# Kernel optimization log

Measured on AMD Instinct MI355X. Metric: run time of the kernel, lower is better.

## Reference

```python
import jax, jax.numpy as jnp
import numpy as np

B, C, H, Wd = 16, 256, 64, 64
D_MODEL = 256


def setup_inputs() -> dict:
    key = jax.random.key(0)
    kx, kw = jax.random.split(key)
    x = jax.random.normal(kx, (B, C, H, Wd), dtype=jnp.float32)
    # 1x1 conv weight [out_c=1+2*d_model, in_c], scaled like kaiming-ish init
    W = jax.random.normal(kw, (1 + 2 * D_MODEL, C), dtype=jnp.float32) / np.sqrt(C)
    return {"x": x, "W": W}


def reference(x, W):
    b, c, h, w = x.shape
    d = (W.shape[0] - 1) // 2
    n = h * w
    xf = x.reshape(b, c, n)                      # [b, c, N]
    qkv = jnp.einsum('oc,bcn->bon', W, xf)       # 1x1 conv == channel GEMM
    q = qkv[:, :1]                               # [b, 1, N]
    k = qkv[:, 1:1 + d]                          # [b, d, N]
    v = qkv[:, 1 + d:]                           # [b, d, N]
    scores = jax.nn.softmax(q, axis=-1)          # softmax over tokens
    ctx = jnp.sum(k * scores, axis=-1, keepdims=True)  # [b, d, 1]
    out = jax.nn.relu(v) * ctx                   # gated ReLU(v)
    return out.reshape(b, d, h, w)
```

## Files before the change

kernel.cpp:

```cpp
#include <hip/hip_runtime.h>
#include <cstdint>
#include <cstddef>

#define NB 16
#define NC 256
#define NN 4096
#define ND 256

typedef unsigned short u16;
typedef unsigned int u32;

typedef __attribute__((ext_vector_type(8))) short short8;
typedef __attribute__((ext_vector_type(4))) float f32x4;

__device__ __forceinline__ u16 f2bf(float f) {
  union { float f; u32 u; } v; v.f = f;
  u32 r = v.u + 0x7FFFu + ((v.u >> 16) & 1u);
  return (u16)(r >> 16);
}
__device__ __forceinline__ float bf2f(u16 h) {
  union { u32 u; float f; } v; v.u = ((u32)h) << 16; return v.f;
}

__global__ __launch_bounds__(256) void k_fuse1(const float* __restrict__ x,
                                               const float* __restrict__ W,
                                               u16* __restrict__ xbT,
                                               u16* __restrict__ wvb,
                                               float* __restrict__ pm,
                                               float* __restrict__ pl,
                                               float* __restrict__ pacc) {
  __shared__ float qred[32 * 65];
  __shared__ float qred2[4 * 65];
  const int t = threadIdx.x;
  const int b = blockIdx.y, n0 = blockIdx.x * 64;
  const int tx = t & 7, ty = t >> 3;
  const int c0 = ty * 8, nl = tx * 8;
  const float* xb = x + (size_t)b * NC * NN + n0;

  const float4 w0 = *(const float4*)(W + c0);
  const float4 w1 = *(const float4*)(W + c0 + 4);
  const float wq[8] = {w0.x, w0.y, w0.z, w0.w, w1.x, w1.y, w1.z, w1.w};

  short8 pk[8];
  float qp[8] = {0.f, 0.f, 0.f, 0.f, 0.f, 0.f, 0.f, 0.f};

#pragma unroll
  for (int r = 0; r < 8; ++r) {
    const float* xr = xb + (size_t)(c0 + r) * NN + nl;
    const float4 va = *(const float4*)(xr);
    const float4 vb = *(const float4*)(xr + 4);
    qp[0] += wq[r] * va.x; qp[1] += wq[r] * va.y;
    qp[2] += wq[r] * va.z; qp[3] += wq[r] * va.w;
    qp[4] += wq[r] * vb.x; qp[5] += wq[r] * vb.y;
    qp[6] += wq[r] * vb.z; qp[7] += wq[r] * vb.w;
    pk[0][r] = (short)f2bf(va.x); pk[1][r] = (short)f2bf(va.y);
    pk[2][r] = (short)f2bf(va.z); pk[3][r] = (short)f2bf(va.w);
    pk[4][r] = (short)f2bf(vb.x); pk[5][r] = (short)f2bf(vb.y);
    pk[6][r] = (short)f2bf(vb.z); pk[7][r] = (short)f2bf(vb.w);
  }

  u16* ob = xbT + (size_t)(b * NN + n0 + nl) * NC + c0;
#pragma unroll
  for (int j = 0; j < 8; ++j)
    *(short8*)(ob + (size_t)j * NC) = pk[j];

#pragma unroll
  for (int j = 0; j < 8; ++j) qred[ty * 65 + nl + j] = qp[j];
  __syncthreads();
  {
    const int n = t & 63, g = t >> 6;
    float s = 0.f;
#pragma unroll
    for (int k = 0; k < 8; ++k) s += qred[(g * 8 + k) * 65 + n];
    qred2[g * 65 + n] = s;
  }
  __syncthreads();

  float q[8];
#pragma unroll
  for (int j = 0; j < 8; ++j)
    q[j] = qred2[0 * 65 + nl + j] + qred2[1 * 65 + nl + j] +
           qred2[2 * 65 + nl + j] + qred2[3 * 65 + nl + j];

  float m = q[0];
#pragma unroll
  for (int j = 1; j < 8; ++j) m = fmaxf(m, q[j]);
#pragma unroll
  for (int off = 1; off < 8; off <<= 1) m = fmaxf(m, __shfl_xor(m, off));

  float p[8]; float l = 0.f;
#pragma unroll
  for (int j = 0; j < 8; ++j) { p[j] = __expf(q[j] - m); l += p[j]; }
#pragma unroll
  for (int off = 1; off < 8; off <<= 1) l += __shfl_xor(l, off);

  float sc[8];
#pragma unroll
  for (int r = 0; r < 8; ++r) {
    float s = 0.f;
#pragma unroll
    for (int j = 0; j < 8; ++j) s += bf2f((u16)pk[j][r]) * p[j];
    sc[r] = s;
  }
#pragma unroll
  for (int off = 1; off < 8; off <<= 1) {
#pragma unroll
    for (int r = 0; r < 8; ++r) sc[r] += __shfl_xor(sc[r], off);
  }
  if (tx == 0) {
    float* pp = pacc + ((size_t)b * 64 + blockIdx.x) * NC + c0;
#pragma unroll
    for (int r = 0; r < 8; ++r) pp[r] = sc[r];
  }
  if (t == 0) {
    pm[b * 64 + blockIdx.x] = m;
    pl[b * 64 + blockIdx.x] = l;
  }

  if (b == 0 && blockIdx.x < 8) {
    const float* wv = W + (size_t)(1 + ND) * NC;
    const int base = blockIdx.x * 8192;
#pragma unroll
    for (int i = 0; i < 8; ++i) {
      const int idx = base + i * 1024 + t * 4;
      const float4 v = *(const float4*)(wv + idx);
      ushort4 o = {f2bf(v.x), f2bf(v.y), f2bf(v.z), f2bf(v.w)};
      *(ushort4*)(wvb + idx) = o;
    }
  }
}

#define BM 128
#define BN 128
#define BK 64

__global__ __launch_bounds__(256, 4) void k_gemm(const u16* __restrict__ xbT,
                                                 const u16* __restrict__ wvb,
                                                 const float* __restrict__ W,
                                                 const float* __restrict__ pm,
                                                 const float* __restrict__ pl,
                                                 const float* __restrict__ pacc,
                                                 float* __restrict__ out) {
  __shared__ __align__(16) u16 As[BM * BK];
  __shared__ __align__(16) u16 Bs[BN * BK];
  __shared__ float am[64], al[64];
  __shared__ __align__(16) float sx[NC];
  __shared__ float sctx[NC];

  const int t = threadIdx.x;
  const int d0 = blockIdx.x * BM;
  const int n0 = blockIdx.y * BN;
  const int b = blockIdx.z;
  const int lane = t & 63, w = t >> 6;
  const int wd = (w & 1) * 64, wn = (w >> 1) * 64;
  const int quad = lane >> 4, l15 = lane & 15;

  const int rstg = t >> 3;
  const int l8 = ((t & 7) ^ (rstg & 7)) * 8;
  const u16* gA = wvb + (size_t)(d0 + rstg) * NC + l8;
  const u16* gB = xbT + (size_t)(b * NN + n0 + rstg) * NC + l8;
  const int ldst = 8 * t;

#pragma unroll
  for (int i = 0; i < 4; ++i) {
    __builtin_amdgcn_global_load_lds(
        (const __attribute__((address_space(1))) u32*)(gA + (size_t)(32 * i) * NC),
        (__attribute__((address_space(3))) u32*)(As + 2048 * i + ldst), 16, 0, 0);
    __builtin_amdgcn_global_load_lds(
        (const __attribute__((address_space(1))) u32*)(gB + (size_t)(32 * i) * NC),
        (__attribute__((address_space(3))) u32*)(Bs + 2048 * i + ldst), 16, 0, 0);
  }

  if (t < 64) { am[t] = pm[b * 64 + t]; al[t] = pl[b * 64 + t]; }
  __syncthreads();
  float M2 = -3.4e38f;
#pragma unroll
  for (int i = 0; i < 64; ++i) M2 = fmaxf(M2, am[i]);
  {
    float xsv = 0.f, L2s = 0.f;
#pragma unroll 8
    for (int i = 0; i < 64; ++i) {
      const float wgt = __expf(am[i] - M2);
      L2s += wgt * al[i];
      xsv += wgt * pacc[(size_t)(b * 64 + i) * NC + t];
    }
    sx[t] = xsv / L2s;
  }
  __syncthreads();
  {
    const float* wk = W + (size_t)(1 + t) * NC;
    float a = 0.f;
#pragma unroll 4
    for (int c4 = 0; c4 < 64; ++c4) {
      const float4 w4 = *(const float4*)(wk + c4 * 4);
      const float4 s4 = *(const float4*)&sx[c4 * 4];
      a += w4.x * s4.x + w4.y * s4.y + w4.z * s4.z + w4.w * s4.w;
    }
    sctx[t] = a;
  }

  f32x4 acc[4][4];
#pragma unroll
  for (int ni = 0; ni < 4; ++ni)
#pragma unroll
    for (int mi = 0; mi < 4; ++mi)
      acc[ni][mi] = (f32x4){0.f, 0.f, 0.f, 0.f};

  const int pq0 = ((0 * 4 + quad) ^ (l15 & 7)) * 8;
  const int pq1 = ((1 * 4 + quad) ^ (l15 & 7)) * 8;

  for (int kk = 0; kk < NC; kk += BK) {
    if (kk) {
      __syncthreads();
#pragma unroll
      for (int i = 0; i < 4; ++i) {
        __builtin_amdgcn_global_load_lds(
            (const __attribute__((address_space(1))) u32*)(gA + kk + (size_t)(32 * i) * NC),
            (__attribute__((address_space(3))) u32*)(As + 2048 * i + ldst), 16, 0, 0);
        __builtin_amdgcn_global_load_lds(
            (const __attribute__((address_space(1))) u32*)(gB + kk + (size_t)(32 * i) * NC),
            (__attribute__((address_space(3))) u32*)(Bs + 2048 * i + ldst), 16, 0, 0);
      }
    }
    __syncthreads();

#pragma unroll
    for (int kq = 0; kq < 2; ++kq) {
      const int pq = kq ? pq1 : pq0;
      short8 xf[4], wf[4];
#pragma unroll
      for (int ni = 0; ni < 4; ++ni)
        xf[ni] = *(const short8*)&Bs[(wn + ni * 16 + l15) * BK + pq];
#pragma unroll
      for (int mi = 0; mi < 4; ++mi)
        wf[mi] = *(const short8*)&As[(wd + mi * 16 + l15) * BK + pq];
#pragma unroll
      for (int ni = 0; ni < 4; ++ni)
#pragma unroll
        for (int mi = 0; mi < 4; ++mi)
          acc[ni][mi] = __builtin_amdgcn_mfma_f32_16x16x32_bf16(xf[ni], wf[mi],
                                                                acc[ni][mi], 0, 0, 0);
    }
  }

#pragma unroll
  for (int mi = 0; mi < 4; ++mi) {
    const int d = d0 + wd + mi * 16 + l15;
    const float cx = sctx[d];
    float* op = out + (size_t)(b * NC + d) * NN + n0 + wn + quad * 4;
#pragma unroll
    for (int ni = 0; ni < 4; ++ni) {
      f32x4 v = acc[ni][mi];
      v[0] = fmaxf(v[0], 0.f) * cx;
      v[1] = fmaxf(v[1], 0.f) * cx;
      v[2] = fmaxf(v[2], 0.f) * cx;
      v[3] = fmaxf(v[3], 0.f) * cx;
      __builtin_nontemporal_store(v, (f32x4*)(op + ni * 16));
    }
  }
}

extern "C" void kernel_launch(void* const* d_in, const int* in_sizes, int n_in,
                              void* d_out, int out_size, void* d_ws, size_t ws_size,
                              hipStream_t stream) {
  const float* x = (const float*)d_in[0];
  const float* W = (const float*)d_in[1];
  float* out = (float*)d_out;

  char* ws = (char*)d_ws;
  u16* xbT    = (u16*)ws;
  float* pacc = (float*)(ws + 33554432);
  float* pm   = (float*)(ws + 34603008);
  float* pl   = (float*)(ws + 34607104);
  u16* wvb    = (u16*)(ws + 34611200);

  k_fuse1<<<dim3(64, 16), 256, 0, stream>>>(x, W, xbT, wvb, pm, pl, pacc);
  k_gemm<<<dim3(2, 32, 16), 256, 0, stream>>>(xbT, wvb, W, pm, pl, pacc, out);
}
```

Baseline: 173.7 us.

## Hoist per-batch softmax combine and ctx GEMV into a separate small kernel

The per-batch softmax merge and the ctx = Wk·x_weighted GEMV were recomputed redundantly by all 64 GEMM blocks of each batch. This moves that work into a new k_combine kernel of 16 blocks that writes ctx to workspace. The GEMM then just reads ctx in its epilogue, drops the related shared memory and raises its occupancy hint to 5. The cost is one extra kernel launch and a serial dependency, and the GEMM prologue no longer overlaps the first tile load with that computation.

```diff
diff --git a/kernel.cpp b/kernel.cpp
--- a/kernel.cpp
+++ b/kernel.cpp
@@ -130,22 +130,50 @@
   }
 }
 
+__global__ __launch_bounds__(256) void k_combine(const float* __restrict__ W,
+                                                 const float* __restrict__ pm,
+                                                 const float* __restrict__ pl,
+                                                 const float* __restrict__ pacc,
+                                                 float* __restrict__ ctx) {
+  __shared__ float sm[64], sl[64], sw[64];
+  __shared__ __align__(16) float sx[NC];
+  const int b = blockIdx.x, t = threadIdx.x;
+  if (t < 64) { sm[t] = pm[b * 64 + t]; sl[t] = pl[b * 64 + t]; }
+  __syncthreads();
+  float M = -3.4e38f;
+#pragma unroll 16
+  for (int i = 0; i < 64; ++i) M = fmaxf(M, sm[i]);
+  if (t < 64) sw[t] = __expf(sm[t] - M);
+  __syncthreads();
+  float L = 0.f;
+#pragma unroll 16
+  for (int i = 0; i < 64; ++i) L += sw[i] * sl[i];
+  float xsc = 0.f;
+#pragma unroll 8
+  for (int i = 0; i < 64; ++i) xsc += sw[i] * pacc[((size_t)b * 64 + i) * NC + t];
+  sx[t] = xsc / L;
+  __syncthreads();
+  const float* wk = W + (size_t)(1 + t) * NC;
+  float a = 0.f;
+#pragma unroll 4
+  for (int c4 = 0; c4 < 64; ++c4) {
+    const float4 w4 = *(const float4*)(wk + c4 * 4);
+    const float4 s4 = *(const float4*)&sx[c4 * 4];
+    a += w4.x * s4.x + w4.y * s4.y + w4.z * s4.z + w4.w * s4.w;
+  }
+  ctx[b * NC + t] = a;
+}
+
 #define BM 128
 #define BN 128
 #define BK 64
 
-__global__ __launch_bounds__(256, 4) void k_gemm(const u16* __restrict__ xbT,
+__global__ __launch_bounds__(256, 5) void k_gemm(const u16* __restrict__ xbT,
                                                  const u16* __restrict__ wvb,
-                                                 const float* __restrict__ W,
-                                                 const float* __restrict__ pm,
-                                                 const float* __restrict__ pl,
-                                                 const float* __restrict__ pacc,
+                                                 const float* __restrict__ ctx,
                                                  float* __restrict__ out) {
   __shared__ __align__(16) u16 As[BM * BK];
   __shared__ __align__(16) u16 Bs[BN * BK];
-  __shared__ float am[64], al[64];
-  __shared__ __align__(16) float sx[NC];
-  __shared__ float sctx[NC];
 
   const int t = threadIdx.x;
   const int d0 = blockIdx.x * BM;
@@ -161,44 +189,6 @@
   const u16* gB = xbT + (size_t)(b * NN + n0 + rstg) * NC + l8;
   const int ldst = 8 * t;
 
-#pragma unroll
-  for (int i = 0; i < 4; ++i) {
-    __builtin_amdgcn_global_load_lds(
-        (const __attribute__((address_space(1))) u32*)(gA + (size_t)(32 * i) * NC),
-        (__attribute__((address_space(3))) u32*)(As + 2048 * i + ldst), 16, 0, 0);
-    __builtin_amdgcn_global_load_lds(
-        (const __attribute__((address_space(1))) u32*)(gB + (size_t)(32 * i) * NC),
-        (__attribute__((address_space(3))) u32*)(Bs + 2048 * i + ldst), 16, 0, 0);
-  }
-
-  if (t < 64) { am[t] = pm[b * 64 + t]; al[t] = pl[b * 64 + t]; }
-  __syncthreads();
-  float M2 = -3.4e38f;
-#pragma unroll
-  for (int i = 0; i < 64; ++i) M2 = fmaxf(M2, am[i]);
-  {
-    float xsv = 0.f, L2s = 0.f;
-#pragma unroll 8
-    for (int i = 0; i < 64; ++i) {
-      const float wgt = __expf(am[i] - M2);
-      L2s += wgt * al[i];
-      xsv += wgt * pacc[(size_t)(b * 64 + i) * NC + t];
-    }
-    sx[t] = xsv / L2s;
-  }
-  __syncthreads();
-  {
-    const float* wk = W + (size_t)(1 + t) * NC;
-    float a = 0.f;
-#pragma unroll 4
-    for (int c4 = 0; c4 < 64; ++c4) {
-      const float4 w4 = *(const float4*)(wk + c4 * 4);
-      const float4 s4 = *(const float4*)&sx[c4 * 4];
-      a += w4.x * s4.x + w4.y * s4.y + w4.z * s4.z + w4.w * s4.w;
-    }
-    sctx[t] = a;
-  }
-
   f32x4 acc[4][4];
 #pragma unroll
   for (int ni = 0; ni < 4; ++ni)
@@ -210,17 +200,15 @@
   const int pq1 = ((1 * 4 + quad) ^ (l15 & 7)) * 8;
 
   for (int kk = 0; kk < NC; kk += BK) {
-    if (kk) {
-      __syncthreads();
-#pragma unroll
-      for (int i = 0; i < 4; ++i) {
-        __builtin_amdgcn_global_load_lds(
-            (const __attribute__((address_space(1))) u32*)(gA + kk + (size_t)(32 * i) * NC),
-            (__attribute__((address_space(3))) u32*)(As + 2048 * i + ldst), 16, 0, 0);
-        __builtin_amdgcn_global_load_lds(
-            (const __attribute__((address_space(1))) u32*)(gB + kk + (size_t)(32 * i) * NC),
-            (__attribute__((address_space(3))) u32*)(Bs + 2048 * i + ldst), 16, 0, 0);
-      }
+    if (kk) __syncthreads();
+#pragma unroll
+    for (int i = 0; i < 4; ++i) {
+      __builtin_amdgcn_global_load_lds(
+          (const __attribute__((address_space(1))) u32*)(gA + kk + (size_t)(32 * i) * NC),
+          (__attribute__((address_space(3))) u32*)(As + 2048 * i + ldst), 16, 0, 0);
+      __builtin_amdgcn_global_load_lds(
+          (const __attribute__((address_space(1))) u32*)(gB + kk + (size_t)(32 * i) * NC),
+          (__attribute__((address_space(3))) u32*)(Bs + 2048 * i + ldst), 16, 0, 0);
     }
     __syncthreads();
 
@@ -246,7 +234,7 @@
 #pragma unroll
   for (int mi = 0; mi < 4; ++mi) {
     const int d = d0 + wd + mi * 16 + l15;
-    const float cx = sctx[d];
+    const float cx = ctx[b * NC + d];
     float* op = out + (size_t)(b * NC + d) * NN + n0 + wn + quad * 4;
 #pragma unroll
     for (int ni = 0; ni < 4; ++ni) {
@@ -272,8 +260,10 @@
   float* pacc = (float*)(ws + 33554432);
   float* pm   = (float*)(ws + 34603008);
   float* pl   = (float*)(ws + 34607104);
-  u16* wvb    = (u16*)(ws + 34611200);
+  float* ctxb = (float*)(ws + 34611200);
+  u16* wvb    = (u16*)(ws + 34627584);
 
   k_fuse1<<<dim3(64, 16), 256, 0, stream>>>(x, W, xbT, wvb, pm, pl, pacc);
-  k_gemm<<<dim3(2, 32, 16), 256, 0, stream>>>(xbT, wvb, W, pm, pl, pacc, out);
-}
+  k_combine<<<16, 256, 0, stream>>>(W, pm, pl, pacc, ctxb);
+  k_gemm<<<dim3(2, 32, 16), 256, 0, stream>>>(xbT, wvb, ctxb, out);
+}
```

Result: slower. 195.3 us (+12.4%).
